# Kernel tuning notes

Hardware: AMD Instinct MI355X
Metric: run time of the kernel (lower is better)

Reference implementation:

```python
import jax, jax.numpy as jnp
import numpy as np

N_NODES = 100000
INPUT_DIM = 512
OUTPUT_DIM = 128
N_EDGES = 300000


def setup_inputs() -> dict:
    key = jax.random.key(0)
    k1, k2, k3, k4, k5 = jax.random.split(key, 5)
    x = jax.random.normal(k1, (N_NODES, INPUT_DIM), dtype=jnp.float32)
    train_edges = jax.random.randint(k2, (N_EDGES, 2), 0, N_NODES, dtype=jnp.int64)
    train_false_edges = jax.random.randint(k3, (N_EDGES, 2), 0, N_NODES, dtype=jnp.int64)
    # learned params (xavier / kaiming init approximated with uniform fan-based scales)
    limit_w = float(np.sqrt(6.0 / (INPUT_DIM + OUTPUT_DIM)))
    weight = jax.random.uniform(k4, (INPUT_DIM, OUTPUT_DIM), dtype=jnp.float32,
                                minval=-limit_w, maxval=limit_w)
    limit_w3 = float(np.sqrt(6.0 / OUTPUT_DIM) / np.sqrt(2.0))
    weight_three = jax.random.uniform(k5, (OUTPUT_DIM, 1), dtype=jnp.float32,
                                      minval=-limit_w3, maxval=limit_w3)
    return {"x": x, "train_edges": train_edges, "train_false_edges": train_false_edges,
            "weight": weight, "weight_three": weight_three}


def _decode(z, edges, weight_three):
    # gather endpoints, elementwise multiply, matvec against weight_three
    prod = z[edges[:, 0]] * z[edges[:, 1]]  # [E, output_dim]
    return prod @ weight_three               # [E, 1]


def reference(x, train_edges, train_false_edges, weight, weight_three):
    z = x @ weight  # encode: [N, output_dim]
    z1 = _decode(z, train_edges, weight_three)
    z2 = _decode(z, train_false_edges, weight_three)
    return jax.nn.sigmoid(jnp.concatenate((z1, z2), axis=0))
```

## Files before the change

### kernel.cpp

```cpp
#include <hip/hip_runtime.h>
#include <math.h>

#define IN_DIM 512
#define OUT_DIM 128
#define BM 64
#define BK 64
#define NKT (IN_DIM / BK)

typedef __attribute__((ext_vector_type(8))) __bf16 bf16x8;
typedef __attribute__((ext_vector_type(4))) float f32x4;
typedef __attribute__((ext_vector_type(2))) float f32x2;

__device__ inline unsigned short f2bf(float f) {
    unsigned u = __float_as_uint(f);
    u += 0x7FFFu + ((u >> 16) & 1u);
    return (unsigned short)(u >> 16);
}
__device__ inline unsigned pack2f(float a, float b) {
    return (unsigned)f2bf(a) | ((unsigned)f2bf(b) << 16);
}

__device__ inline int swz(int row, int kbyte) {
    return row * 128 + (kbyte ^ ((row & 7) << 4));
}

__global__ void wt2_kernel(const float* __restrict__ w, unsigned short* __restrict__ wt2) {
    int idx = blockIdx.x * 256 + threadIdx.x;
    int k = idx >> 7;
    int n = idx & 127;
    wt2[(((k >> 3) * 128) + n) * 8 + (k & 7)] = f2bf(w[idx]);
}

__global__ __launch_bounds__(256, 6) void gemm_mfma(const float* __restrict__ x,
                                                    const unsigned short* __restrict__ wt2,
                                                    unsigned short* __restrict__ zb,
                                                    int M) {
    __shared__ unsigned short sA[BM * BK];
    char* const pA = (char*)sA;

    const int tid  = threadIdx.x;
    const int lane = tid & 63;
    const int wid  = tid >> 6;
    const int wm   = wid >> 1;
    const int wn   = wid & 1;
    const int block_row = blockIdx.x * BM;

    f32x4 acc[2][4];
#pragma unroll
    for (int i = 0; i < 2; ++i)
#pragma unroll
        for (int j = 0; j < 4; ++j) acc[i][j] = (f32x4){0.f, 0.f, 0.f, 0.f};

    const int a_row = tid >> 2;
    const int a_col = (tid & 3) * 16;
    const bool a_ok = (block_row + a_row) < M;
    const float* xp = x + (size_t)(block_row + a_row) * IN_DIM + a_col;
    const int a_b0 = swz(a_row, a_col * 2);
    const int a_b1 = swz(a_row, a_col * 2 + 16);

    const int fr  = lane & 15;
    const int fk4 = lane >> 4;
    const int fkb = fk4 * 16;

    const unsigned short* wtb = wt2 + (size_t)fk4 * 1024 + (wn * 64 + fr) * 8;

    float4 ra[4];
    const float4 z4 = make_float4(0.f, 0.f, 0.f, 0.f);

#pragma unroll
    for (int i = 0; i < 4; ++i) ra[i] = a_ok ? *(const float4*)(xp + 4 * i) : z4;

#pragma unroll
    for (int kt = 0; kt < NKT; ++kt) {
        if (kt) __syncthreads();
        const float* rf = (const float*)ra;
        uint4 u0, u1;
        u0.x = pack2f(rf[0], rf[1]);   u0.y = pack2f(rf[2], rf[3]);
        u0.z = pack2f(rf[4], rf[5]);   u0.w = pack2f(rf[6], rf[7]);
        u1.x = pack2f(rf[8], rf[9]);   u1.y = pack2f(rf[10], rf[11]);
        u1.z = pack2f(rf[12], rf[13]); u1.w = pack2f(rf[14], rf[15]);
        *(uint4*)(pA + a_b0) = u0;
        *(uint4*)(pA + a_b1) = u1;
        __syncthreads();

        if (kt + 1 < NKT) {
            const int k0 = (kt + 1) * BK;
#pragma unroll
            for (int i = 0; i < 4; ++i)
                ra[i] = a_ok ? *(const float4*)(xp + k0 + 4 * i) : z4;
        }

#pragma unroll
        for (int ks = 0; ks < 2; ++ks) {
            bf16x8 af[2], bv[4];
#pragma unroll
            for (int mf = 0; mf < 2; ++mf)
                af[mf] = *(const bf16x8*)(pA + swz(wm * 32 + mf * 16 + fr, ks * 64 + fkb));
#pragma unroll
            for (int nf = 0; nf < 4; ++nf)
                bv[nf] = *(const bf16x8*)(wtb + kt * 8192 + ks * 4096 + nf * 128);
#pragma unroll
            for (int mf = 0; mf < 2; ++mf)
#pragma unroll
                for (int nf = 0; nf < 4; ++nf)
                    acc[mf][nf] = __builtin_amdgcn_mfma_f32_16x16x32_bf16(
                        af[mf], bv[nf], acc[mf][nf], 0, 0, 0);
        }
    }

    const int crow0 = (lane >> 4) * 4;
    const int ccol  = lane & 15;
#pragma unroll
    for (int mf = 0; mf < 2; ++mf)
#pragma unroll
        for (int r = 0; r < 4; ++r) {
            const int grow = block_row + wm * 32 + mf * 16 + crow0 + r;
            if (grow < M) {
                unsigned short* zr = zb + (size_t)grow * OUT_DIM + wn * 64 + ccol;
#pragma unroll
                for (int nf = 0; nf < 4; ++nf)
                    zr[nf * 16] = f2bf(acc[mf][nf][r]);
            }
        }
}

__device__ inline float dotw3(const uint4& ua, const uint4& ub, const f32x2* w3v) {
    const unsigned pa[4] = {ua.x, ua.y, ua.z, ua.w};
    const unsigned pb[4] = {ub.x, ub.y, ub.z, ub.w};
    f32x2 vv = (f32x2){0.f, 0.f};
#pragma unroll
    for (int i = 0; i < 4; ++i) {
        f32x2 A = (f32x2){__uint_as_float(pa[i] << 16),
                          __uint_as_float(pa[i] & 0xFFFF0000u)};
        f32x2 B = (f32x2){__uint_as_float(pb[i] << 16),
                          __uint_as_float(pb[i] & 0xFFFF0000u)};
        vv += (A * B) * w3v[i];
    }
    return vv.x + vv.y;
}

__global__ __launch_bounds__(256) void decode_kernel(const unsigned short* __restrict__ zb,
                                                     const int* __restrict__ e1,
                                                     const int* __restrict__ e2,
                                                     const float* __restrict__ w3,
                                                     float* __restrict__ out,
                                                     int E1, int E2) {
    const int tid  = threadIdx.x;
    const int lane = tid & 63;
    const int sub  = lane & 15;
    const int sg   = lane >> 4;
    const int Etot = E1 + E2;
    const int nq   = (Etot + 3) >> 2;

    f32x2 w3v[4];
    {
        const float4 wlo = *(const float4*)(w3 + sub * 8);
        const float4 whi = *(const float4*)(w3 + sub * 8 + 4);
        w3v[0] = (f32x2){wlo.x, wlo.y};
        w3v[1] = (f32x2){wlo.z, wlo.w};
        w3v[2] = (f32x2){whi.x, whi.y};
        w3v[3] = (f32x2){whi.z, whi.w};
    }

    const int wave = blockIdx.x * 4 + (tid >> 6);
    const int S    = gridDim.x * 4;

    for (int q = wave; q < nq; q += 2 * S) {
        const int q2   = q + S;
        const bool has2 = (q2 < nq);

        const int e_a = q * 4 + sg;
        const int e_b = has2 ? (q2 * 4 + sg) : e_a;
        const int ca  = min(e_a, Etot - 1);
        const int cb  = min(e_b, Etot - 1);

        const int2 ia = (ca < E1) ? ((const int2*)e1)[ca] : ((const int2*)e2)[ca - E1];
        const int2 ib = (cb < E1) ? ((const int2*)e1)[cb] : ((const int2*)e2)[cb - E1];

        const uint4 a1 = *(const uint4*)(zb + (size_t)ia.x * OUT_DIM + sub * 8);
        const uint4 b1 = *(const uint4*)(zb + (size_t)ia.y * OUT_DIM + sub * 8);
        const uint4 a2 = *(const uint4*)(zb + (size_t)ib.x * OUT_DIM + sub * 8);
        const uint4 b2 = *(const uint4*)(zb + (size_t)ib.y * OUT_DIM + sub * 8);

        float v1 = dotw3(a1, b1, w3v);
        float v2 = dotw3(a2, b2, w3v);

        v1 += __shfl_xor(v1, 8);  v2 += __shfl_xor(v2, 8);
        v1 += __shfl_xor(v1, 4);  v2 += __shfl_xor(v2, 4);
        v1 += __shfl_xor(v1, 2);  v2 += __shfl_xor(v2, 2);
        v1 += __shfl_xor(v1, 1);  v2 += __shfl_xor(v2, 1);

        if (sub == 0) {
            if (e_a < Etot) out[e_a] = 1.f / (1.f + __expf(-v1));
            if (has2 && e_b < Etot) out[e_b] = 1.f / (1.f + __expf(-v2));
        }
    }
}

extern "C" void kernel_launch(void* const* d_in, const int* in_sizes, int n_in,
                              void* d_out, int out_size, void* d_ws, size_t ws_size,
                              hipStream_t stream) {
    const float* x  = (const float*)d_in[0];
    const int*   e1 = (const int*)d_in[1];
    const int*   e2 = (const int*)d_in[2];
    const float* w  = (const float*)d_in[3];
    const float* w3 = (const float*)d_in[4];

    float* out = (float*)d_out;

    const int M  = in_sizes[0] / IN_DIM;
    const int E1 = in_sizes[1] / 2;
    const int E2 = in_sizes[2] / 2;

    unsigned short* zbuf = (unsigned short*)d_ws;
    unsigned short* wt2  = zbuf + (size_t)M * OUT_DIM;

    wt2_kernel<<<(IN_DIM * OUT_DIM) / 256, 256, 0, stream>>>(w, wt2);
    gemm_mfma<<<(M + BM - 1) / BM, 256, 0, stream>>>(x, wt2, zbuf, M);
    decode_kernel<<<2048, 256, 0, stream>>>(zbuf, e1, e2, w3, out, E1, E2);
}
```

Baseline: 101.0 us.

## Load A fragments directly from global memory, drop LDS staging in GEMM

The GEMM no longer stages x tiles through shared memory with barriers. Each wave now loads its A fragments straight from global memory in fp32 and converts them to bf16 in registers with native casts. Out-of-range rows are clamped to the last row instead of zero-filled. This removes the LDS round trip, the bank swizzle and the syncthreads, but the two wn waves now each load the same x rows, doubling global/L2 traffic for x. The software prefetch of the next tile is also lost, and occupancy drops from 6 to 4 blocks per SM.

```diff
diff --git a/kernel.cpp b/kernel.cpp
--- a/kernel.cpp
+++ b/kernel.cpp
@@ -4,10 +4,10 @@
 #define IN_DIM 512
 #define OUT_DIM 128
 #define BM 64
-#define BK 64
-#define NKT (IN_DIM / BK)
+#define NKT (IN_DIM / 64)
 
 typedef __attribute__((ext_vector_type(8))) __bf16 bf16x8;
+typedef __attribute__((ext_vector_type(2))) __bf16 bf16x2;
 typedef __attribute__((ext_vector_type(4))) float f32x4;
 typedef __attribute__((ext_vector_type(2))) float f32x2;
 
@@ -16,12 +16,15 @@
     u += 0x7FFFu + ((u >> 16) & 1u);
     return (unsigned short)(u >> 16);
 }
-__device__ inline unsigned pack2f(float a, float b) {
-    return (unsigned)f2bf(a) | ((unsigned)f2bf(b) << 16);
-}
-
-__device__ inline int swz(int row, int kbyte) {
-    return row * 128 + (kbyte ^ ((row & 7) << 4));
+
+__device__ inline bf16x8 cvt8(const float4& lo, const float4& hi) {
+    bf16x2 p0 = {(__bf16)lo.x, (__bf16)lo.y};
+    bf16x2 p1 = {(__bf16)lo.z, (__bf16)lo.w};
+    bf16x2 p2 = {(__bf16)hi.x, (__bf16)hi.y};
+    bf16x2 p3 = {(__bf16)hi.z, (__bf16)hi.w};
+    uint4 u = {__builtin_bit_cast(unsigned, p0), __builtin_bit_cast(unsigned, p1),
+               __builtin_bit_cast(unsigned, p2), __builtin_bit_cast(unsigned, p3)};
+    return __builtin_bit_cast(bf16x8, u);
 }
 
 __global__ void wt2_kernel(const float* __restrict__ w, unsigned short* __restrict__ wt2) {
@@ -31,13 +34,10 @@
     wt2[(((k >> 3) * 128) + n) * 8 + (k & 7)] = f2bf(w[idx]);
 }
 
-__global__ __launch_bounds__(256, 6) void gemm_mfma(const float* __restrict__ x,
+__global__ __launch_bounds__(256, 4) void gemm_mfma(const float* __restrict__ x,
                                                     const unsigned short* __restrict__ wt2,
                                                     unsigned short* __restrict__ zb,
                                                     int M) {
-    __shared__ unsigned short sA[BM * BK];
-    char* const pA = (char*)sA;
-
     const int tid  = threadIdx.x;
     const int lane = tid & 63;
     const int wid  = tid >> 6;
@@ -45,57 +45,37 @@
     const int wn   = wid & 1;
     const int block_row = blockIdx.x * BM;
 
-    f32x4 acc[2][4];
-#pragma unroll
-    for (int i = 0; i < 2; ++i)
-#pragma unroll
-        for (int j = 0; j < 4; ++j) acc[i][j] = (f32x4){0.f, 0.f, 0.f, 0.f};
-
-    const int a_row = tid >> 2;
-    const int a_col = (tid & 3) * 16;
-    const bool a_ok = (block_row + a_row) < M;
-    const float* xp = x + (size_t)(block_row + a_row) * IN_DIM + a_col;
-    const int a_b0 = swz(a_row, a_col * 2);
-    const int a_b1 = swz(a_row, a_col * 2 + 16);
-
     const int fr  = lane & 15;
     const int fk4 = lane >> 4;
-    const int fkb = fk4 * 16;
-
+
+    f32x4 acc[2][4];
+#pragma unroll
+    for (int i = 0; i < 2; ++i)
+#pragma unroll
+        for (int j = 0; j < 4; ++j) acc[i][j] = (f32x4){0.f, 0.f, 0.f, 0.f};
+
+    const float* xa[2];
+#pragma unroll
+    for (int mf = 0; mf < 2; ++mf) {
+        int r = block_row + wm * 32 + mf * 16 + fr;
+        r = (r < M) ? r : (M - 1);
+        xa[mf] = x + (size_t)r * IN_DIM + fk4 * 8;
+    }
     const unsigned short* wtb = wt2 + (size_t)fk4 * 1024 + (wn * 64 + fr) * 8;
 
-    float4 ra[4];
-    const float4 z4 = make_float4(0.f, 0.f, 0.f, 0.f);
-
-#pragma unroll
-    for (int i = 0; i < 4; ++i) ra[i] = a_ok ? *(const float4*)(xp + 4 * i) : z4;
-
 #pragma unroll
     for (int kt = 0; kt < NKT; ++kt) {
-        if (kt) __syncthreads();
-        const float* rf = (const float*)ra;
-        uint4 u0, u1;
-        u0.x = pack2f(rf[0], rf[1]);   u0.y = pack2f(rf[2], rf[3]);
-        u0.z = pack2f(rf[4], rf[5]);   u0.w = pack2f(rf[6], rf[7]);
-        u1.x = pack2f(rf[8], rf[9]);   u1.y = pack2f(rf[10], rf[11]);
-        u1.z = pack2f(rf[12], rf[13]); u1.w = pack2f(rf[14], rf[15]);
-        *(uint4*)(pA + a_b0) = u0;
-        *(uint4*)(pA + a_b1) = u1;
-        __syncthreads();
-
-        if (kt + 1 < NKT) {
-            const int k0 = (kt + 1) * BK;
-#pragma unroll
-            for (int i = 0; i < 4; ++i)
-                ra[i] = a_ok ? *(const float4*)(xp + k0 + 4 * i) : z4;
-        }
-
 #pragma unroll
         for (int ks = 0; ks < 2; ++ks) {
-            bf16x8 af[2], bv[4];
-#pragma unroll
-            for (int mf = 0; mf < 2; ++mf)
-                af[mf] = *(const bf16x8*)(pA + swz(wm * 32 + mf * 16 + fr, ks * 64 + fkb));
+            const int ko = kt * 64 + ks * 32;
+            bf16x8 af[2];
+#pragma unroll
+            for (int mf = 0; mf < 2; ++mf) {
+                const float4 lo = *(const float4*)(xa[mf] + ko);
+                const float4 hi = *(const float4*)(xa[mf] + ko + 4);
+                af[mf] = cvt8(lo, hi);
+            }
+            bf16x8 bv[4];
 #pragma unroll
             for (int nf = 0; nf < 4; ++nf)
                 bv[nf] = *(const bf16x8*)(wtb + kt * 8192 + ks * 4096 + nf * 128);
@@ -166,7 +146,7 @@
     const int S    = gridDim.x * 4;
 
     for (int q = wave; q < nq; q += 2 * S) {
-        const int q2   = q + S;
+        const int q2    = q + S;
         const bool has2 = (q2 < nq);
 
         const int e_a = q * 4 + sg;
```

Measured after the change: 117.2 us. 1.16x slower.

## Use 512-thread GEMM blocks with one M-fragment per wave and packed stores

Applied to the files above, without the earlier changes.

The encode GEMM block grows from 256 to 512 threads (8 waves), with each wave computing a 16x64 tile instead of 32x64. Each thread loads 8 floats of x per k-tile instead of 16, spreading the global load and bf16 conversion across more waves to hide memory latency. The MFMA operands are swapped so the accumulator layout lets each lane write 4 contiguous bf16 values as a packed 8-byte store instead of scalar 2-byte stores. In exchange, each wave now loads the B fragments from global memory to feed only one M-fragment, doubling B-load traffic per MFMA.

```diff
diff --git a/kernel.cpp b/kernel.cpp
--- a/kernel.cpp
+++ b/kernel.cpp
@@ -31,7 +31,7 @@
     wt2[(((k >> 3) * 128) + n) * 8 + (k & 7)] = f2bf(w[idx]);
 }
 
-__global__ __launch_bounds__(256, 6) void gemm_mfma(const float* __restrict__ x,
+__global__ __launch_bounds__(512, 8) void gemm_mfma(const float* __restrict__ x,
                                                     const unsigned short* __restrict__ wt2,
                                                     unsigned short* __restrict__ zb,
                                                     int M) {
@@ -45,83 +45,72 @@
     const int wn   = wid & 1;
     const int block_row = blockIdx.x * BM;
 
-    f32x4 acc[2][4];
-#pragma unroll
-    for (int i = 0; i < 2; ++i)
-#pragma unroll
-        for (int j = 0; j < 4; ++j) acc[i][j] = (f32x4){0.f, 0.f, 0.f, 0.f};
-
-    const int a_row = tid >> 2;
-    const int a_col = (tid & 3) * 16;
-    const bool a_ok = (block_row + a_row) < M;
-    const float* xp = x + (size_t)(block_row + a_row) * IN_DIM + a_col;
-    const int a_b0 = swz(a_row, a_col * 2);
-    const int a_b1 = swz(a_row, a_col * 2 + 16);
-
     const int fr  = lane & 15;
     const int fk4 = lane >> 4;
     const int fkb = fk4 * 16;
 
-    const unsigned short* wtb = wt2 + (size_t)fk4 * 1024 + (wn * 64 + fr) * 8;
-
-    float4 ra[4];
+    f32x4 acc[4];
+#pragma unroll
+    for (int j = 0; j < 4; ++j) acc[j] = (f32x4){0.f, 0.f, 0.f, 0.f};
+
+    const int a_row = tid >> 3;
+    const int a_col = (tid & 7) * 8;
+    const bool a_ok = (block_row + a_row) < M;
+    const float* xp = x + (size_t)(block_row + a_row) * IN_DIM + a_col;
+    const int a_b = swz(a_row, a_col * 2);
+
+    const unsigned short* pb = wt2 + fk4 * 1024 + (wn * 64 + fr) * 8;
+
+    float4 ra0, ra1;
     const float4 z4 = make_float4(0.f, 0.f, 0.f, 0.f);
 
-#pragma unroll
-    for (int i = 0; i < 4; ++i) ra[i] = a_ok ? *(const float4*)(xp + 4 * i) : z4;
+    ra0 = a_ok ? *(const float4*)(xp + 0) : z4;
+    ra1 = a_ok ? *(const float4*)(xp + 4) : z4;
 
 #pragma unroll
     for (int kt = 0; kt < NKT; ++kt) {
         if (kt) __syncthreads();
-        const float* rf = (const float*)ra;
-        uint4 u0, u1;
-        u0.x = pack2f(rf[0], rf[1]);   u0.y = pack2f(rf[2], rf[3]);
-        u0.z = pack2f(rf[4], rf[5]);   u0.w = pack2f(rf[6], rf[7]);
-        u1.x = pack2f(rf[8], rf[9]);   u1.y = pack2f(rf[10], rf[11]);
-        u1.z = pack2f(rf[12], rf[13]); u1.w = pack2f(rf[14], rf[15]);
-        *(uint4*)(pA + a_b0) = u0;
-        *(uint4*)(pA + a_b1) = u1;
+        uint4 u;
+        u.x = pack2f(ra0.x, ra0.y);
+        u.y = pack2f(ra0.z, ra0.w);
+        u.z = pack2f(ra1.x, ra1.y);
+        u.w = pack2f(ra1.z, ra1.w);
+        *(uint4*)(pA + a_b) = u;
         __syncthreads();
 
         if (kt + 1 < NKT) {
             const int k0 = (kt + 1) * BK;
-#pragma unroll
-            for (int i = 0; i < 4; ++i)
-                ra[i] = a_ok ? *(const float4*)(xp + k0 + 4 * i) : z4;
+            ra0 = a_ok ? *(const float4*)(xp + k0 + 0) : z4;
+            ra1 = a_ok ? *(const float4*)(xp + k0 + 4) : z4;
         }
 
 #pragma unroll
         for (int ks = 0; ks < 2; ++ks) {
-            bf16x8 af[2], bv[4];
-#pragma unroll
-            for (int mf = 0; mf < 2; ++mf)
-                af[mf] = *(const bf16x8*)(pA + swz(wm * 32 + mf * 16 + fr, ks * 64 + fkb));
-#pragma unroll
-            for (int nf = 0; nf < 4; ++nf)
-                bv[nf] = *(const bf16x8*)(wtb + kt * 8192 + ks * 4096 + nf * 128);
-#pragma unroll
-            for (int mf = 0; mf < 2; ++mf)
-#pragma unroll
-                for (int nf = 0; nf < 4; ++nf)
-                    acc[mf][nf] = __builtin_amdgcn_mfma_f32_16x16x32_bf16(
-                        af[mf], bv[nf], acc[mf][nf], 0, 0, 0);
-        }
-    }
-
-    const int crow0 = (lane >> 4) * 4;
-    const int ccol  = lane & 15;
-#pragma unroll
-    for (int mf = 0; mf < 2; ++mf)
-#pragma unroll
-        for (int r = 0; r < 4; ++r) {
-            const int grow = block_row + wm * 32 + mf * 16 + crow0 + r;
-            if (grow < M) {
-                unsigned short* zr = zb + (size_t)grow * OUT_DIM + wn * 64 + ccol;
-#pragma unroll
-                for (int nf = 0; nf < 4; ++nf)
-                    zr[nf * 16] = f2bf(acc[mf][nf][r]);
-            }
-        }
+            const bf16x8 af = *(const bf16x8*)(pA + swz(wm * 16 + fr, ks * 64 + fkb));
+            const bf16x8 bv0 = *(const bf16x8*)(pb + kt * 8192 + ks * 4096 + 0);
+            const bf16x8 bv1 = *(const bf16x8*)(pb + kt * 8192 + ks * 4096 + 128);
+            const bf16x8 bv2 = *(const bf16x8*)(pb + kt * 8192 + ks * 4096 + 256);
+            const bf16x8 bv3 = *(const bf16x8*)(pb + kt * 8192 + ks * 4096 + 384);
+            acc[0] = __builtin_amdgcn_mfma_f32_16x16x32_bf16(bv0, af, acc[0], 0, 0, 0);
+            acc[1] = __builtin_amdgcn_mfma_f32_16x16x32_bf16(bv1, af, acc[1], 0, 0, 0);
+            acc[2] = __builtin_amdgcn_mfma_f32_16x16x32_bf16(bv2, af, acc[2], 0, 0, 0);
+            acc[3] = __builtin_amdgcn_mfma_f32_16x16x32_bf16(bv3, af, acc[3], 0, 0, 0);
+        }
+    }
+
+    const int cm  = lane & 15;
+    const int cn0 = (lane >> 4) * 4;
+    const int grow = block_row + wm * 16 + cm;
+    if (grow < M) {
+        unsigned short* zr = zb + (size_t)grow * OUT_DIM + wn * 64 + cn0;
+#pragma unroll
+        for (int nf = 0; nf < 4; ++nf) {
+            uint2 u;
+            u.x = pack2f(acc[nf][0], acc[nf][1]);
+            u.y = pack2f(acc[nf][2], acc[nf][3]);
+            *(uint2*)(zr + nf * 16) = u;
+        }
+    }
 }
 
 __device__ inline float dotw3(const uint4& ua, const uint4& ub, const f32x2* w3v) {
@@ -166,7 +155,7 @@
     const int S    = gridDim.x * 4;
 
     for (int q = wave; q < nq; q += 2 * S) {
-        const int q2   = q + S;
+        const int q2    = q + S;
         const bool has2 = (q2 < nq);
 
         const int e_a = q * 4 + sg;
@@ -216,6 +205,6 @@
     unsigned short* wt2  = zbuf + (size_t)M * OUT_DIM;
 
     wt2_kernel<<<(IN_DIM * OUT_DIM) / 256, 256, 0, stream>>>(w, wt2);
-    gemm_mfma<<<(M + BM - 1) / BM, 256, 0, stream>>>(x, wt2, zbuf, M);
+    gemm_mfma<<<(M + BM - 1) / BM, 512, 0, stream>>>(x, wt2, zbuf, M);
     decode_kernel<<<2048, 256, 0, stream>>>(zbuf, e1, e2, w3, out, E1, E2);
 }
```

Result: slower. 178.7 us (+77.0%).
